# Kernel tuning notes

Hardware: AMD Instinct MI355X
Metric: run time of the kernel (lower is better)

The kernel has to match this reference:

```python
import jax, jax.numpy as jnp
import numpy as np

N_HEADS = 16

def setup_inputs() -> dict:
    key = jax.random.key(0)
    qkv = jax.random.normal(key, (4, 3072, 2048), dtype=jnp.float32)
    return {"qkv": qkv}

def reference(qkv) -> jnp.ndarray:
    bs, width, length = qkv.shape
    ch = width // (3 * N_HEADS)
    # [bs*H, 3*ch, T] -> split into q, k, v each [bs*H, ch, T]
    qkv_r = qkv.reshape(bs * N_HEADS, 3 * ch, length)
    q, k, v = qkv_r[:, :ch], qkv_r[:, ch:2 * ch], qkv_r[:, 2 * ch:]
    scale = 1.0 / jnp.sqrt(jnp.sqrt(jnp.float32(ch)))
    # scores: [bs*H, T, T]
    weight = jnp.einsum('bct,bcs->bts', q * scale, k * scale)
    weight = jax.nn.softmax(weight.astype(jnp.float32), axis=-1).astype(weight.dtype)
    a = jnp.einsum('bts,bcs->bct', weight, v)  # [bs*H, ch, T]
    return a.reshape(bs, N_HEADS * ch, length)
```

## Files before the change

### kernel.cpp

```cpp
#include <hip/hip_runtime.h>

namespace {

constexpr int D  = 64;
constexpr int T  = 2048;
constexpr int TQ = 64;
constexpr int NT = T / 64;
constexpr float SCL = 0.125f * 1.44269504088896340736f;

constexpr size_t QP_OFF  = (size_t)64 * 32 * 8192;
constexpr size_t WS_NEED = ((size_t)64 * 32 * 8192 + (size_t)64 * 32 * 4096) * 2;

typedef __bf16 bf16x8 __attribute__((ext_vector_type(8)));
typedef float  f32x4  __attribute__((ext_vector_type(4)));
typedef unsigned short u16x4 __attribute__((ext_vector_type(4)));
typedef unsigned short u16x8 __attribute__((ext_vector_type(8)));
typedef unsigned int   u32x2 __attribute__((ext_vector_type(2)));
typedef short          s16x4 __attribute__((ext_vector_type(4)));

__device__ inline unsigned short f2bf(float f) {
    unsigned int u = __builtin_bit_cast(unsigned int, f);
    u += 0x7FFFu + ((u >> 16) & 1u);
    return (unsigned short)(u >> 16);
}

__device__ inline unsigned int pkbf(float a, float b) {
#if __has_builtin(__builtin_amdgcn_cvt_pk_bf16_f32)
    auto r = __builtin_amdgcn_cvt_pk_bf16_f32(a, b);
    static_assert(sizeof(r) == 4, "cvt_pk_bf16 size");
    return __builtin_bit_cast(unsigned int, r);
#else
    return (unsigned int)f2bf(a) | ((unsigned int)f2bf(b) << 16);
#endif
}

__device__ inline int frag_off(int row, int c0) {
    int g = (c0 >> 3) ^ ((row >> 1) & 7);
    return row * 64 + g * 8;
}

__device__ inline void async_cp16(const void* g, void* l) {
    __builtin_amdgcn_global_load_lds(
        (const __attribute__((address_space(1))) unsigned int*)g,
        (__attribute__((address_space(3))) unsigned int*)l, 16, 0, 0);
}

__global__ __launch_bounds__(256)
void prepass(const float* __restrict__ qkv, unsigned short* __restrict__ ws) {
    const int tile = blockIdx.x, h = blockIdx.y, z = blockIdx.z;
    const int tid = threadIdx.x;
    const float* src = qkv + (size_t)h * 3 * D * T + (size_t)z * D * T + tile * 64;
    __shared__ unsigned short L[4096];

    if (z == 2) {
        unsigned short* dst = ws + (size_t)(h * 32 + tile) * 8192 + 4096;
        const int c = tid >> 2, g = tid & 3;
        const int sg = g ^ ((c >> 2) & 3);
        #pragma unroll
        for (int wq = 0; wq < 4; wq++) {
            f32x4 a = *(const f32x4*)(src + (size_t)c * T + wq * 16 + sg * 4);
            u16x4 wv = { f2bf(a[0]), f2bf(a[1]), f2bf(a[2]), f2bf(a[3]) };
            *(u16x4*)(dst + wq * 1024 + tid * 4) = wv;
        }
    } else {
        const float m = (z == 0) ? SCL : 1.0f;
        const int c0 = (tid >> 4) * 4, s4 = tid & 15;
        float fr[4][4];
        #pragma unroll
        for (int r = 0; r < 4; r++)
            *(f32x4*)fr[r] = *(const f32x4*)(src + (size_t)(c0 + r) * T + s4 * 4);
        #pragma unroll
        for (int j = 0; j < 4; j++) {
            int trow = s4 * 4 + j;
            u16x4 wv = { f2bf(fr[0][j] * m), f2bf(fr[1][j] * m),
                         f2bf(fr[2][j] * m), f2bf(fr[3][j] * m) };
            *(u16x4*)(L + frag_off(trow, c0) + (c0 & 7)) = wv;
        }
        __syncthreads();
        unsigned short* dst = (z == 0)
            ? ws + QP_OFF + (size_t)(h * 32 + tile) * 4096
            : ws + (size_t)(h * 32 + tile) * 8192;
        #pragma unroll
        for (int i = 0; i < 2; i++)
            *(u16x8*)(dst + tid * 16 + i * 8) = *(const u16x8*)(L + tid * 16 + i * 8);
    }
}


#define STAGE(J, B)                                                          \
  { const char* g = kvb + (size_t)(J) * 16384;                               \
    char* lk = wbase + (B) * 4096;                                           \
    async_cp16(g,               lk);                                         \
    async_cp16(g + 1024,        lk + 1024);                                  \
    async_cp16(g + 8192,        lk + 2048);                                  \
    async_cp16(g + 8192 + 1024, lk + 3072); }

#define BODY(KT, B, DO_STAGE, WAITIMM)                                       \
  {                                                                          \
    __builtin_amdgcn_s_waitcnt(0xC07F);           \
    if (DO_STAGE) STAGE((KT) + 1, (B) ^ 1)                                   \
    __builtin_amdgcn_s_waitcnt(WAITIMM);       \
    bf16x8 aK0 = *(const bf16x8*)aKp[B][0];                                  \
    bf16x8 aK1 = *(const bf16x8*)aKp[B][1];                                  \
    s16x4 aV0 = *(const s16x4*)aVp[B][0];                                    \
    s16x4 aV1 = *(const s16x4*)aVp[B][1];                                    \
    s16x4 aV2 = *(const s16x4*)aVp[B][2];                                    \
    s16x4 aV3 = *(const s16x4*)aVp[B][3];                                    \
    f32x4 acc_s[4];                                                          \
    _Pragma("unroll")                                                        \
    for (int ti = 0; ti < 4; ti++)                                           \
      acc_s[ti] = __builtin_amdgcn_mfma_f32_16x16x32_bf16(                   \
          aK0, bQ[ti][0], ZF, 0, 0, 0);                                      \
    _Pragma("unroll")                                                        \
    for (int ti = 0; ti < 4; ti++)                                           \
      acc_s[ti] = __builtin_amdgcn_mfma_f32_16x16x32_bf16(                   \
          aK1, bQ[ti][1], acc_s[ti], 0, 0, 0);                               \
    s16x4 bP[4];                                                             \
    _Pragma("unroll")                                                        \
    for (int ti = 0; ti < 4; ti++) {                                         \
      float p0 = __builtin_amdgcn_exp2f(acc_s[ti][0]);                       \
      float p1 = __builtin_amdgcn_exp2f(acc_s[ti][1]);                       \
      float p2 = __builtin_amdgcn_exp2f(acc_s[ti][2]);                       \
      float p3 = __builtin_amdgcn_exp2f(acc_s[ti][3]);                       \
      l_acc[ti] += (p0 + p1) + (p2 + p3);                                    \
      u32x2 pk = { pkbf(p0, p1), pkbf(p2, p3) };                             \
      bP[ti] = __builtin_bit_cast(s16x4, pk);                                \
    }                                                                        \
    _Pragma("unroll")                                                        \
    for (int ti = 0; ti < 4; ti++) {                                         \
      acc_o[0][ti] = __builtin_amdgcn_mfma_f32_16x16x16bf16_1k(              \
          aV0, bP[ti], acc_o[0][ti], 0, 0, 0);                               \
      acc_o[1][ti] = __builtin_amdgcn_mfma_f32_16x16x16bf16_1k(              \
          aV1, bP[ti], acc_o[1][ti], 0, 0, 0);                               \
      acc_o[2][ti] = __builtin_amdgcn_mfma_f32_16x16x16bf16_1k(              \
          aV2, bP[ti], acc_o[2][ti], 0, 0, 0);                               \
      acc_o[3][ti] = __builtin_amdgcn_mfma_f32_16x16x16bf16_1k(              \
          aV3, bP[ti], acc_o[3][ti], 0, 0, 0);                               \
    }                                                                        \
  }

__global__ __launch_bounds__(256, 3)
void attn_main(const unsigned short* __restrict__ ws, float* __restrict__ out) {
    const int h  = blockIdx.x;
    const int qt = blockIdx.y;
    const int t0 = qt * TQ;
    const int tid  = threadIdx.x;
    const int lane = tid & 63;
    const int w    = tid >> 6;
    const int ln   = lane & 15, q4 = lane >> 4;

    __shared__ char  sbuf[32768];
    __shared__ float lbuf[256];
    char* wbase = sbuf + w * 8192;

    const unsigned short* qtile = ws + QP_OFF + (size_t)(h * 32 + qt) * 4096;
    bf16x8 bQ[4][2];
    #pragma unroll
    for (int ti = 0; ti < 4; ti++)
        #pragma unroll
        for (int kc = 0; kc < 2; kc++)
            bQ[ti][kc] = *(const bf16x8*)(qtile + frag_off(ti * 16 + ln, kc * 32 + q4 * 8));

    const unsigned short* aKp[2][2];
    const unsigned short* aVp[2][4];
    const int vsw = (q4 ^ ((ln >> 2) & 3)) * 4;
    #pragma unroll
    for (int b = 0; b < 2; b++) {
        const unsigned short* base = (const unsigned short*)(wbase + b * 4096);
        #pragma unroll
        for (int kc = 0; kc < 2; kc++)
            aKp[b][kc] = base + frag_off(ln, kc * 32 + q4 * 8);
        #pragma unroll
        for (int ci = 0; ci < 4; ci++)
            aVp[b][ci] = base + 1024 + (16 * ci + ln) * 16 + vsw;
    }
    const char* kvb = (const char*)ws + (size_t)(h * 32) * 16384
                      + (size_t)w * 2048 + lane * 16;
    const f32x4 ZF = {0.f, 0.f, 0.f, 0.f};

    f32x4 acc_o[4][4];
    #pragma unroll
    for (int ci = 0; ci < 4; ci++)
        #pragma unroll
        for (int ti = 0; ti < 4; ti++) acc_o[ci][ti] = ZF;
    float l_acc[4] = {0.f, 0.f, 0.f, 0.f};

    STAGE(0, 0)

    #pragma unroll 1
    for (int m = 0; m < 15; m++) {
        BODY(2 * m,     0, 1, 0x0F74)
        BODY(2 * m + 1, 1, 1, 0x0F74)
    }
    BODY(30, 0, 1, 0x0F74)
    BODY(31, 1, 0, 0x0F70)

    __syncthreads();
    #pragma unroll
    for (int ti = 0; ti < 4; ti++) {
        float s = l_acc[ti];
        s += __shfl_xor(s, 16, 64);
        s += __shfl_xor(s, 32, 64);
        if (q4 == 0) lbuf[w * 64 + ti * 16 + ln] = s;
    }
    float* slots = (float*)sbuf;
    #pragma unroll
    for (int q = 0; q < 4; q++)
        if ((q ^ w) & 1) {
            float* dst = slots + w * 2048 + (q >> 1) * 1024;
            #pragma unroll
            for (int ti = 0; ti < 4; ti++)
                *(f32x4*)(dst + ti * 256 + lane * 4) = acc_o[q][ti];
        }
    __syncthreads();
    #pragma unroll
    for (int q = 0; q < 4; q++)
        if (!((q ^ w) & 1)) {
            const float* srcp = slots + (w ^ 1) * 2048 + (q >> 1) * 1024;
            #pragma unroll
            for (int ti = 0; ti < 4; ti++)
                acc_o[q][ti] += *(const f32x4*)(srcp + ti * 256 + lane * 4);
        }
    __syncthreads();
    #pragma unroll
    for (int q = 0; q < 4; q++)
        if (((q ^ w) & 3) == 2) {
            float* dst = slots + w * 2048;
            #pragma unroll
            for (int ti = 0; ti < 4; ti++)
                *(f32x4*)(dst + ti * 256 + lane * 4) = acc_o[q][ti];
        }
    __syncthreads();
    #pragma unroll
    for (int q = 0; q < 4; q++)
        if (q == w) {
            const float* srcp = slots + (w ^ 2) * 2048;
            float linv[4];
            #pragma unroll
            for (int ti = 0; ti < 4; ti++) {
                int tt = ti * 16 + ln;
                linv[ti] = 1.0f / (lbuf[tt] + lbuf[64 + tt] +
                                   lbuf[128 + tt] + lbuf[192 + tt]);
                acc_o[q][ti] += *(const f32x4*)(srcp + ti * 256 + lane * 4);
            }
            float* ob = out + (size_t)h * D * T + t0;
            #pragma unroll
            for (int ti = 0; ti < 4; ti++)
                #pragma unroll
                for (int rr = 0; rr < 4; rr++) {
                    int c = 16 * w + q4 * 4 + rr;
                    ob[(size_t)c * T + ti * 16 + ln] = acc_o[q][ti][rr] * linv[ti];
                }
        }
}

__device__ inline bf16x8 frag8(const unsigned short* p, int row, int c0) {
    return *(const bf16x8*)(p + frag_off(row, c0));
}

__global__ __launch_bounds__(256)
void attn_fallback(const float* __restrict__ qkv, float* __restrict__ out) {
    const int h     = blockIdx.y;
    const int t0    = blockIdx.x * TQ;
    const int tid   = threadIdx.x;
    const int lane  = tid & 63;
    const int strip = tid >> 6;
    const int ln    = lane & 15;
    const int q4    = lane >> 4;

    __shared__ unsigned short Qs[TQ * D];
    __shared__ unsigned short Ks[64 * D];
    __shared__ unsigned short Vs[D * 64];
    __shared__ unsigned short Pss[TQ * 64];
    __shared__ float l_lds[TQ];

    const float* qb = qkv + (size_t)h * 3 * D * T;
    const float* kb = qb + (size_t)D * T;
    const float* vb = qb + (size_t)(2 * D) * T;
    const int s4 = tid & 15;
    const int c0 = (tid >> 4) * 4;
    {
        float fr[4][4];
        #pragma unroll
        for (int r = 0; r < 4; r++)
            *(f32x4*)fr[r] = *(const f32x4*)(qb + (size_t)(c0 + r) * T + t0 + s4 * 4);
        #pragma unroll
        for (int j = 0; j < 4; j++) {
            int trow = s4 * 4 + j;
            u16x4 wv = { f2bf(fr[0][j]), f2bf(fr[1][j]), f2bf(fr[2][j]), f2bf(fr[3][j]) };
            *(u16x4*)(Qs + frag_off(trow, c0) + (c0 & 7)) = wv;
        }
    }
    __syncthreads();
    const int arow = strip * 16 + ln;
    const int kg   = q4 * 8;
    const bf16x8 aq0 = frag8(Qs, arow, kg);
    const bf16x8 aq1 = frag8(Qs, arow, 32 + kg);
    f32x4 acc_o[4];
    #pragma unroll
    for (int m = 0; m < 4; m++) acc_o[m] = (f32x4){0.f, 0.f, 0.f, 0.f};
    float l_acc[4] = {0.f, 0.f, 0.f, 0.f};
    constexpr float S2 = 0.125f * 1.44269504088896340736f;
    for (int kt = 0; kt < NT; kt++) {
        const int s0 = kt * 64;
        float kr[4][4], vr[4][4];
        #pragma unroll
        for (int r = 0; r < 4; r++)
            *(f32x4*)kr[r] = *(const f32x4*)(kb + (size_t)(c0 + r) * T + s0 + s4 * 4);
        #pragma unroll
        for (int r = 0; r < 4; r++)
            *(f32x4*)vr[r] = *(const f32x4*)(vb + (size_t)(c0 + r) * T + s0 + s4 * 4);
        __syncthreads();
        #pragma unroll
        for (int j = 0; j < 4; j++) {
            int srow = s4 * 4 + j;
            u16x4 wk = { f2bf(kr[0][j]), f2bf(kr[1][j]), f2bf(kr[2][j]), f2bf(kr[3][j]) };
            *(u16x4*)(Ks + frag_off(srow, c0) + (c0 & 7)) = wk;
        }
        #pragma unroll
        for (int r = 0; r < 4; r++) {
            int row = c0 + r, cc = s4 * 4;
            u16x4 wv = { f2bf(vr[r][0]), f2bf(vr[r][1]), f2bf(vr[r][2]), f2bf(vr[r][3]) };
            *(u16x4*)(Vs + frag_off(row, cc) + (cc & 7)) = wv;
        }
        __syncthreads();
        f32x4 accs[4];
        #pragma unroll
        for (int ns = 0; ns < 4; ns++) {
            bf16x8 b0 = frag8(Ks, ns * 16 + ln, kg);
            bf16x8 b1 = frag8(Ks, ns * 16 + ln, 32 + kg);
            f32x4 z = {0.f, 0.f, 0.f, 0.f};
            z = __builtin_amdgcn_mfma_f32_16x16x32_bf16(aq0, b0, z, 0, 0, 0);
            z = __builtin_amdgcn_mfma_f32_16x16x32_bf16(aq1, b1, z, 0, 0, 0);
            accs[ns] = z;
        }
        #pragma unroll
        for (int ns = 0; ns < 4; ns++) {
            int scol = ns * 16 + ln;
            #pragma unroll
            for (int r = 0; r < 4; r++) {
                float p = __builtin_amdgcn_exp2f(accs[ns][r] * S2);
                l_acc[r] += p;
                int trow = strip * 16 + q4 * 4 + r;
                int g = ((scol >> 3) ^ ((trow >> 1) & 7));
                Pss[trow * 64 + g * 8 + (scol & 7)] = f2bf(p);
            }
        }
        bf16x8 bp0 = frag8(Pss, arow, kg);
        bf16x8 bp1 = frag8(Pss, arow, 32 + kg);
        #pragma unroll
        for (int ms = 0; ms < 4; ms++) {
            bf16x8 av0 = frag8(Vs, ms * 16 + ln, kg);
            bf16x8 av1 = frag8(Vs, ms * 16 + ln, 32 + kg);
            acc_o[ms] = __builtin_amdgcn_mfma_f32_16x16x32_bf16(av0, bp0, acc_o[ms], 0, 0, 0);
            acc_o[ms] = __builtin_amdgcn_mfma_f32_16x16x32_bf16(av1, bp1, acc_o[ms], 0, 0, 0);
        }
    }
    #pragma unroll
    for (int r = 0; r < 4; r++) {
        float s = l_acc[r];
        s += __shfl_xor(s, 1, 64);
        s += __shfl_xor(s, 2, 64);
        s += __shfl_xor(s, 4, 64);
        s += __shfl_xor(s, 8, 64);
        if (ln == 0) l_lds[strip * 16 + q4 * 4 + r] = s;
    }
    const float linv = 1.0f / l_lds[strip * 16 + ln];
    const int tg = t0 + strip * 16 + ln;
    float* ob = out + (size_t)h * D * T;
    #pragma unroll
    for (int ms = 0; ms < 4; ms++)
        #pragma unroll
        for (int r = 0; r < 4; r++) {
            int c = ms * 16 + q4 * 4 + r;
            ob[(size_t)c * T + tg] = acc_o[ms][r] * linv;
        }
}

}

extern "C" void kernel_launch(void* const* d_in, const int* in_sizes, int n_in,
                              void* d_out, int out_size, void* d_ws, size_t ws_size,
                              hipStream_t stream) {
    const float* qkv = (const float*)d_in[0];
    float* out = (float*)d_out;
    if (ws_size >= WS_NEED) {
        prepass<<<dim3(32, 64, 3), 256, 0, stream>>>(qkv, (unsigned short*)d_ws);
        attn_main<<<dim3(64, 32), 256, 0, stream>>>((const unsigned short*)d_ws, out);
    } else {
        attn_fallback<<<dim3(32, 64), 256, 0, stream>>>(qkv, out);
    }
}
```

Measured before the change: 254.3 us.

## Load Q directly in attention kernel and deepen K/V prefetch pipeline

The prepass no longer converts Q. The attention kernel now loads its Q tile from fp32 input, scales and converts it to bf16, and stages it through shared memory, which removes a workspace round-trip and one third of the prepass grid. The K/V loop now issues global-to-LDS copies two tiles ahead and register-prefetches the next tile's fragments. It also interleaves the QK MFMA, exp and PV MFMA per pair of query subtiles, with a sched_barrier in between. The row-sum buffer is folded into the reused shared slots, at the cost of more register pressure and harder occupancy at 3 waves/SIMD.

```diff
diff --git a/kernel.cpp b/kernel.cpp
--- a/kernel.cpp
+++ b/kernel.cpp
@@ -8,8 +8,7 @@
 constexpr int NT = T / 64;
 constexpr float SCL = 0.125f * 1.44269504088896340736f;
 
-constexpr size_t QP_OFF  = (size_t)64 * 32 * 8192;
-constexpr size_t WS_NEED = ((size_t)64 * 32 * 8192 + (size_t)64 * 32 * 4096) * 2;
+constexpr size_t WS_NEED = (size_t)64 * 32 * 8192 * 2;
 
 typedef __bf16 bf16x8 __attribute__((ext_vector_type(8)));
 typedef float  f32x4  __attribute__((ext_vector_type(4)));
@@ -47,12 +46,12 @@
 
 __global__ __launch_bounds__(256)
 void prepass(const float* __restrict__ qkv, unsigned short* __restrict__ ws) {
-    const int tile = blockIdx.x, h = blockIdx.y, z = blockIdx.z;
+    const int tile = blockIdx.x, h = blockIdx.y, zz = blockIdx.z;
     const int tid = threadIdx.x;
-    const float* src = qkv + (size_t)h * 3 * D * T + (size_t)z * D * T + tile * 64;
+    const float* src = qkv + (size_t)h * 3 * D * T + (size_t)(zz + 1) * D * T + tile * 64;
     __shared__ unsigned short L[4096];
 
-    if (z == 2) {
+    if (zz == 1) {
         unsigned short* dst = ws + (size_t)(h * 32 + tile) * 8192 + 4096;
         const int c = tid >> 2, g = tid & 3;
         const int sg = g ^ ((c >> 2) & 3);
@@ -63,7 +62,6 @@
             *(u16x4*)(dst + wq * 1024 + tid * 4) = wv;
         }
     } else {
-        const float m = (z == 0) ? SCL : 1.0f;
         const int c0 = (tid >> 4) * 4, s4 = tid & 15;
         float fr[4][4];
         #pragma unroll
@@ -72,14 +70,12 @@
         #pragma unroll
         for (int j = 0; j < 4; j++) {
             int trow = s4 * 4 + j;
-            u16x4 wv = { f2bf(fr[0][j] * m), f2bf(fr[1][j] * m),
-                         f2bf(fr[2][j] * m), f2bf(fr[3][j] * m) };
+            u16x4 wv = { f2bf(fr[0][j]), f2bf(fr[1][j]),
+                         f2bf(fr[2][j]), f2bf(fr[3][j]) };
             *(u16x4*)(L + frag_off(trow, c0) + (c0 & 7)) = wv;
         }
         __syncthreads();
-        unsigned short* dst = (z == 0)
-            ? ws + QP_OFF + (size_t)(h * 32 + tile) * 4096
-            : ws + (size_t)(h * 32 + tile) * 8192;
+        unsigned short* dst = ws + (size_t)(h * 32 + tile) * 8192;
         #pragma unroll
         for (int i = 0; i < 2; i++)
             *(u16x8*)(dst + tid * 16 + i * 8) = *(const u16x8*)(L + tid * 16 + i * 8);
@@ -95,52 +91,65 @@
     async_cp16(g + 8192,        lk + 2048);                                  \
     async_cp16(g + 8192 + 1024, lk + 3072); }
 
-#define BODY(KT, B, DO_STAGE, WAITIMM)                                       \
+#define PREF(NB)                                                             \
+  { aK[NB][0] = *(const bf16x8*)(wbase + (NB) * 4096 + kOff0);               \
+    aK[NB][1] = *(const bf16x8*)(wbase + (NB) * 4096 + kOff1);               \
+    aV[NB][0] = *(const s16x4*)(wbase + (NB) * 4096 + vBase);                \
+    aV[NB][1] = *(const s16x4*)(wbase + (NB) * 4096 + vBase + 512);          \
+    aV[NB][2] = *(const s16x4*)(wbase + (NB) * 4096 + vBase + 1024);         \
+    aV[NB][3] = *(const s16x4*)(wbase + (NB) * 4096 + vBase + 1536); }
+
+#define BODY(KT, B, DO_STAGE, DO_PREF, WAITIMM)                              \
   {                                                                          \
     __builtin_amdgcn_s_waitcnt(0xC07F);           \
-    if (DO_STAGE) STAGE((KT) + 1, (B) ^ 1)                                   \
-    __builtin_amdgcn_s_waitcnt(WAITIMM);       \
-    bf16x8 aK0 = *(const bf16x8*)aKp[B][0];                                  \
-    bf16x8 aK1 = *(const bf16x8*)aKp[B][1];                                  \
-    s16x4 aV0 = *(const s16x4*)aVp[B][0];                                    \
-    s16x4 aV1 = *(const s16x4*)aVp[B][1];                                    \
-    s16x4 aV2 = *(const s16x4*)aVp[B][2];                                    \
-    s16x4 aV3 = *(const s16x4*)aVp[B][3];                                    \
-    f32x4 acc_s[4];                                                          \
+    if (DO_STAGE) STAGE((KT) + 2, B)                                         \
+    if (DO_PREF) {                                                           \
+      __builtin_amdgcn_s_waitcnt(WAITIMM);   \
+      PREF((B) ^ 1)                                                          \
+    }                                                                        \
+    __builtin_amdgcn_sched_barrier(0);   \
     _Pragma("unroll")                                                        \
-    for (int ti = 0; ti < 4; ti++)                                           \
-      acc_s[ti] = __builtin_amdgcn_mfma_f32_16x16x32_bf16(                   \
-          aK0, bQ[ti][0], ZF, 0, 0, 0);                                      \
-    _Pragma("unroll")                                                        \
-    for (int ti = 0; ti < 4; ti++)                                           \
-      acc_s[ti] = __builtin_amdgcn_mfma_f32_16x16x32_bf16(                   \
-          aK1, bQ[ti][1], acc_s[ti], 0, 0, 0);                               \
-    s16x4 bP[4];                                                             \
-    _Pragma("unroll")                                                        \
-    for (int ti = 0; ti < 4; ti++) {                                         \
-      float p0 = __builtin_amdgcn_exp2f(acc_s[ti][0]);                       \
-      float p1 = __builtin_amdgcn_exp2f(acc_s[ti][1]);                       \
-      float p2 = __builtin_amdgcn_exp2f(acc_s[ti][2]);                       \
-      float p3 = __builtin_amdgcn_exp2f(acc_s[ti][3]);                       \
-      l_acc[ti] += (p0 + p1) + (p2 + p3);                                    \
-      u32x2 pk = { pkbf(p0, p1), pkbf(p2, p3) };                             \
-      bP[ti] = __builtin_bit_cast(s16x4, pk);                                \
-    }                                                                        \
-    _Pragma("unroll")                                                        \
-    for (int ti = 0; ti < 4; ti++) {                                         \
-      acc_o[0][ti] = __builtin_amdgcn_mfma_f32_16x16x16bf16_1k(              \
-          aV0, bP[ti], acc_o[0][ti], 0, 0, 0);                               \
-      acc_o[1][ti] = __builtin_amdgcn_mfma_f32_16x16x16bf16_1k(              \
-          aV1, bP[ti], acc_o[1][ti], 0, 0, 0);                               \
-      acc_o[2][ti] = __builtin_amdgcn_mfma_f32_16x16x16bf16_1k(              \
-          aV2, bP[ti], acc_o[2][ti], 0, 0, 0);                               \
-      acc_o[3][ti] = __builtin_amdgcn_mfma_f32_16x16x16bf16_1k(              \
-          aV3, bP[ti], acc_o[3][ti], 0, 0, 0);                               \
+    for (int tp = 0; tp < 2; tp++) {     \
+      f32x4 s0 = __builtin_amdgcn_mfma_f32_16x16x32_bf16(                    \
+          aK[B][0], bQ[2 * tp][0], ZF, 0, 0, 0);                             \
+      s0 = __builtin_amdgcn_mfma_f32_16x16x32_bf16(                          \
+          aK[B][1], bQ[2 * tp][1], s0, 0, 0, 0);                             \
+      f32x4 s1 = __builtin_amdgcn_mfma_f32_16x16x32_bf16(                    \
+          aK[B][0], bQ[2 * tp + 1][0], ZF, 0, 0, 0);                         \
+      s1 = __builtin_amdgcn_mfma_f32_16x16x32_bf16(                          \
+          aK[B][1], bQ[2 * tp + 1][1], s1, 0, 0, 0);                         \
+      s16x4 bP0, bP1;                                                        \
+      {                                                                      \
+        float p0 = __builtin_amdgcn_exp2f(s0[0]);                            \
+        float p1 = __builtin_amdgcn_exp2f(s0[1]);                            \
+        float p2 = __builtin_amdgcn_exp2f(s0[2]);                            \
+        float p3 = __builtin_amdgcn_exp2f(s0[3]);                            \
+        l_acc[2 * tp] += (p0 + p1) + (p2 + p3);                              \
+        u32x2 pk = { pkbf(p0, p1), pkbf(p2, p3) };                           \
+        bP0 = __builtin_bit_cast(s16x4, pk);                                 \
+      }                                                                      \
+      {                                                                      \
+        float p0 = __builtin_amdgcn_exp2f(s1[0]);                            \
+        float p1 = __builtin_amdgcn_exp2f(s1[1]);                            \
+        float p2 = __builtin_amdgcn_exp2f(s1[2]);                            \
+        float p3 = __builtin_amdgcn_exp2f(s1[3]);                            \
+        l_acc[2 * tp + 1] += (p0 + p1) + (p2 + p3);                          \
+        u32x2 pk = { pkbf(p0, p1), pkbf(p2, p3) };                           \
+        bP1 = __builtin_bit_cast(s16x4, pk);                                 \
+      }                                                                      \
+      _Pragma("unroll")                                                      \
+      for (int ci = 0; ci < 4; ci++) {                                       \
+        acc_o[ci][2 * tp]     = __builtin_amdgcn_mfma_f32_16x16x16bf16_1k(   \
+            aV[B][ci], bP0, acc_o[ci][2 * tp], 0, 0, 0);                     \
+        acc_o[ci][2 * tp + 1] = __builtin_amdgcn_mfma_f32_16x16x16bf16_1k(   \
+            aV[B][ci], bP1, acc_o[ci][2 * tp + 1], 0, 0, 0);                 \
+      }                                                                      \
     }                                                                        \
   }
 
 __global__ __launch_bounds__(256, 3)
-void attn_main(const unsigned short* __restrict__ ws, float* __restrict__ out) {
+void attn_main(const unsigned short* __restrict__ ws,
+               const float* __restrict__ qkv, float* __restrict__ out) {
     const int h  = blockIdx.x;
     const int qt = blockIdx.y;
     const int t0 = qt * TQ;
@@ -149,35 +158,47 @@
     const int w    = tid >> 6;
     const int ln   = lane & 15, q4 = lane >> 4;
 
-    __shared__ char  sbuf[32768];
-    __shared__ float lbuf[256];
+    __shared__ char sbuf[32768];
     char* wbase = sbuf + w * 8192;
-
-    const unsigned short* qtile = ws + QP_OFF + (size_t)(h * 32 + qt) * 4096;
-    bf16x8 bQ[4][2];
-    #pragma unroll
-    for (int ti = 0; ti < 4; ti++)
-        #pragma unroll
-        for (int kc = 0; kc < 2; kc++)
-            bQ[ti][kc] = *(const bf16x8*)(qtile + frag_off(ti * 16 + ln, kc * 32 + q4 * 8));
-
-    const unsigned short* aKp[2][2];
-    const unsigned short* aVp[2][4];
-    const int vsw = (q4 ^ ((ln >> 2) & 3)) * 4;
-    #pragma unroll
-    for (int b = 0; b < 2; b++) {
-        const unsigned short* base = (const unsigned short*)(wbase + b * 4096);
-        #pragma unroll
-        for (int kc = 0; kc < 2; kc++)
-            aKp[b][kc] = base + frag_off(ln, kc * 32 + q4 * 8);
-        #pragma unroll
-        for (int ci = 0; ci < 4; ci++)
-            aVp[b][ci] = base + 1024 + (16 * ci + ln) * 16 + vsw;
-    }
+    unsigned short* S16 = (unsigned short*)sbuf;
+
+    const float* qsrc = qkv + (size_t)h * 3 * D * T + t0;
+    const int c0 = (tid >> 4) * 4, s4 = tid & 15;
+    float fr[4][4];
+    #pragma unroll
+    for (int r = 0; r < 4; r++)
+        *(f32x4*)fr[r] = *(const f32x4*)(qsrc + (size_t)(c0 + r) * T + s4 * 4);
+
     const char* kvb = (const char*)ws + (size_t)(h * 32) * 16384
                       + (size_t)w * 2048 + lane * 16;
+    STAGE(0, 0)
+
+    #pragma unroll
+    for (int j = 0; j < 4; j++) {
+        int trow = s4 * 4 + j;
+        int g = (c0 >> 3) ^ ((trow >> 1) & 7);
+        u16x4 wv = { f2bf(fr[0][j] * SCL), f2bf(fr[1][j] * SCL),
+                     f2bf(fr[2][j] * SCL), f2bf(fr[3][j] * SCL) };
+        *(u16x4*)(S16 + (trow >> 4) * 4096 + 2048 + (trow & 15) * 64 + g * 8 + (c0 & 7)) = wv;
+    }
+    __syncthreads();
+    bf16x8 bQ[4][2];
+    #pragma unroll
+    for (int ti = 0; ti < 4; ti++)
+        #pragma unroll
+        for (int kc = 0; kc < 2; kc++) {
+            int cc = kc * 32 + q4 * 8;
+            int g = (cc >> 3) ^ ((ln >> 1) & 7);
+            bQ[ti][kc] = *(const bf16x8*)(S16 + ti * 4096 + 2048 + ln * 64 + g * 8);
+        }
+    __syncthreads();
+
+    const int kOff0 = 2 * frag_off(ln, q4 * 8);
+    const int kOff1 = 2 * frag_off(ln, 32 + q4 * 8);
+    const int vsw   = (q4 ^ ((ln >> 2) & 3)) * 4;
+    const int vBase = 2048 + 32 * ln + 2 * vsw;
+
     const f32x4 ZF = {0.f, 0.f, 0.f, 0.f};
-
     f32x4 acc_o[4][4];
     #pragma unroll
     for (int ci = 0; ci < 4; ci++)
@@ -185,24 +206,28 @@
         for (int ti = 0; ti < 4; ti++) acc_o[ci][ti] = ZF;
     float l_acc[4] = {0.f, 0.f, 0.f, 0.f};
 
-    STAGE(0, 0)
+    bf16x8 aK[2][2];
+    s16x4  aV[2][4];
+    PREF(0)
+    STAGE(1, 1)
 
     #pragma unroll 1
     for (int m = 0; m < 15; m++) {
-        BODY(2 * m,     0, 1, 0x0F74)
-        BODY(2 * m + 1, 1, 1, 0x0F74)
-    }
-    BODY(30, 0, 1, 0x0F74)
-    BODY(31, 1, 0, 0x0F70)
-
-    __syncthreads();
+        BODY(2 * m,     0, 1, 1, 0x0F74)
+        BODY(2 * m + 1, 1, 1, 1, 0x0F74)
+    }
+    BODY(30, 0, 0, 1, 0x0F70)
+    BODY(31, 1, 0, 0, 0x0F70)
+
+    float lv[4];
     #pragma unroll
     for (int ti = 0; ti < 4; ti++) {
         float s = l_acc[ti];
         s += __shfl_xor(s, 16, 64);
         s += __shfl_xor(s, 32, 64);
-        if (q4 == 0) lbuf[w * 64 + ti * 16 + ln] = s;
-    }
+        lv[ti] = s;
+    }
+    __syncthreads();
     float* slots = (float*)sbuf;
     #pragma unroll
     for (int q = 0; q < 4; q++)
@@ -230,6 +255,11 @@
             for (int ti = 0; ti < 4; ti++)
                 *(f32x4*)(dst + ti * 256 + lane * 4) = acc_o[q][ti];
         }
+    if (q4 == 0) {
+        #pragma unroll
+        for (int ti = 0; ti < 4; ti++)
+            slots[w * 2048 + 1024 + ti * 16 + ln] = lv[ti];
+    }
     __syncthreads();
     #pragma unroll
     for (int q = 0; q < 4; q++)
@@ -239,8 +269,8 @@
             #pragma unroll
             for (int ti = 0; ti < 4; ti++) {
                 int tt = ti * 16 + ln;
-                linv[ti] = 1.0f / (lbuf[tt] + lbuf[64 + tt] +
-                                   lbuf[128 + tt] + lbuf[192 + tt]);
+                linv[ti] = 1.0f / (slots[1024 + tt] + slots[2048 + 1024 + tt] +
+                                   slots[4096 + 1024 + tt] + slots[6144 + 1024 + tt]);
                 acc_o[q][ti] += *(const f32x4*)(srcp + ti * 256 + lane * 4);
             }
             float* ob = out + (size_t)h * D * T + t0;
@@ -385,8 +415,8 @@
     const float* qkv = (const float*)d_in[0];
     float* out = (float*)d_out;
     if (ws_size >= WS_NEED) {
-        prepass<<<dim3(32, 64, 3), 256, 0, stream>>>(qkv, (unsigned short*)d_ws);
-        attn_main<<<dim3(64, 32), 256, 0, stream>>>((const unsigned short*)d_ws, out);
+        prepass<<<dim3(32, 64, 2), 256, 0, stream>>>(qkv, (unsigned short*)d_ws);
+        attn_main<<<dim3(64, 32), 256, 0, stream>>>((const unsigned short*)d_ws, qkv, out);
     } else {
         attn_fallback<<<dim3(32, 64), 256, 0, stream>>>(qkv, out);
     }
```

Measured after the change: 293.5 us. 1.15x slower.

## Fuse Q conversion into attention kernel and triple-buffer K/V staging

Applied to the files above, without the earlier changes.

The prepass no longer converts Q to bf16. Instead, attn_main loads its fp32 Q tile directly, scales and converts it, and moves it into registers through LDS. This removes a third of the prepass work and the Q workspace round trip. The K/V async staging also goes from double to triple buffering, prefetching two tiles ahead, which raises LDS to 48KB per block and may limit occupancy under the 3-blocks launch bound.

```diff
diff --git a/kernel.cpp b/kernel.cpp
--- a/kernel.cpp
+++ b/kernel.cpp
@@ -8,8 +8,7 @@
 constexpr int NT = T / 64;
 constexpr float SCL = 0.125f * 1.44269504088896340736f;
 
-constexpr size_t QP_OFF  = (size_t)64 * 32 * 8192;
-constexpr size_t WS_NEED = ((size_t)64 * 32 * 8192 + (size_t)64 * 32 * 4096) * 2;
+constexpr size_t WS_NEED = (size_t)64 * 32 * 8192 * 2;
 
 typedef __bf16 bf16x8 __attribute__((ext_vector_type(8)));
 typedef float  f32x4  __attribute__((ext_vector_type(4)));
@@ -47,12 +46,12 @@
 
 __global__ __launch_bounds__(256)
 void prepass(const float* __restrict__ qkv, unsigned short* __restrict__ ws) {
-    const int tile = blockIdx.x, h = blockIdx.y, z = blockIdx.z;
+    const int tile = blockIdx.x, h = blockIdx.y, zz = blockIdx.z;
     const int tid = threadIdx.x;
-    const float* src = qkv + (size_t)h * 3 * D * T + (size_t)z * D * T + tile * 64;
+    const float* src = qkv + (size_t)h * 3 * D * T + (size_t)(zz + 1) * D * T + tile * 64;
     __shared__ unsigned short L[4096];
 
-    if (z == 2) {
+    if (zz == 1) {
         unsigned short* dst = ws + (size_t)(h * 32 + tile) * 8192 + 4096;
         const int c = tid >> 2, g = tid & 3;
         const int sg = g ^ ((c >> 2) & 3);
@@ -63,7 +62,6 @@
             *(u16x4*)(dst + wq * 1024 + tid * 4) = wv;
         }
     } else {
-        const float m = (z == 0) ? SCL : 1.0f;
         const int c0 = (tid >> 4) * 4, s4 = tid & 15;
         float fr[4][4];
         #pragma unroll
@@ -72,14 +70,12 @@
         #pragma unroll
         for (int j = 0; j < 4; j++) {
             int trow = s4 * 4 + j;
-            u16x4 wv = { f2bf(fr[0][j] * m), f2bf(fr[1][j] * m),
-                         f2bf(fr[2][j] * m), f2bf(fr[3][j] * m) };
+            u16x4 wv = { f2bf(fr[0][j]), f2bf(fr[1][j]),
+                         f2bf(fr[2][j]), f2bf(fr[3][j]) };
             *(u16x4*)(L + frag_off(trow, c0) + (c0 & 7)) = wv;
         }
         __syncthreads();
-        unsigned short* dst = (z == 0)
-            ? ws + QP_OFF + (size_t)(h * 32 + tile) * 4096
-            : ws + (size_t)(h * 32 + tile) * 8192;
+        unsigned short* dst = ws + (size_t)(h * 32 + tile) * 8192;
         #pragma unroll
         for (int i = 0; i < 2; i++)
             *(u16x8*)(dst + tid * 16 + i * 8) = *(const u16x8*)(L + tid * 16 + i * 8);
@@ -95,17 +91,17 @@
     async_cp16(g + 8192,        lk + 2048);                                  \
     async_cp16(g + 8192 + 1024, lk + 3072); }
 
-#define BODY(KT, B, DO_STAGE, WAITIMM)                                       \
+#define BODY(KT, B, SB, DO_STAGE, WAITIMM)                                   \
   {                                                                          \
     __builtin_amdgcn_s_waitcnt(0xC07F);           \
-    if (DO_STAGE) STAGE((KT) + 1, (B) ^ 1)                                   \
+    if (DO_STAGE) STAGE((KT) + 2, SB)                                        \
     __builtin_amdgcn_s_waitcnt(WAITIMM);       \
-    bf16x8 aK0 = *(const bf16x8*)aKp[B][0];                                  \
-    bf16x8 aK1 = *(const bf16x8*)aKp[B][1];                                  \
-    s16x4 aV0 = *(const s16x4*)aVp[B][0];                                    \
-    s16x4 aV1 = *(const s16x4*)aVp[B][1];                                    \
-    s16x4 aV2 = *(const s16x4*)aVp[B][2];                                    \
-    s16x4 aV3 = *(const s16x4*)aVp[B][3];                                    \
+    bf16x8 aK0 = *(const bf16x8*)(aK0p + (B) * 4096);                        \
+    bf16x8 aK1 = *(const bf16x8*)(aK1p + (B) * 4096);                        \
+    s16x4 aV0 = *(const s16x4*)(aVp + (B) * 4096);                           \
+    s16x4 aV1 = *(const s16x4*)(aVp + (B) * 4096 + 512);                     \
+    s16x4 aV2 = *(const s16x4*)(aVp + (B) * 4096 + 1024);                    \
+    s16x4 aV3 = *(const s16x4*)(aVp + (B) * 4096 + 1536);                    \
     f32x4 acc_s[4];                                                          \
     _Pragma("unroll")                                                        \
     for (int ti = 0; ti < 4; ti++)                                           \
@@ -140,7 +136,8 @@
   }
 
 __global__ __launch_bounds__(256, 3)
-void attn_main(const unsigned short* __restrict__ ws, float* __restrict__ out) {
+void attn_main(const unsigned short* __restrict__ ws,
+               const float* __restrict__ qkv, float* __restrict__ out) {
     const int h  = blockIdx.x;
     const int qt = blockIdx.y;
     const int t0 = qt * TQ;
@@ -149,35 +146,48 @@
     const int w    = tid >> 6;
     const int ln   = lane & 15, q4 = lane >> 4;
 
-    __shared__ char  sbuf[32768];
-    __shared__ float lbuf[256];
-    char* wbase = sbuf + w * 8192;
-
-    const unsigned short* qtile = ws + QP_OFF + (size_t)(h * 32 + qt) * 4096;
-    bf16x8 bQ[4][2];
-    #pragma unroll
-    for (int ti = 0; ti < 4; ti++)
-        #pragma unroll
-        for (int kc = 0; kc < 2; kc++)
-            bQ[ti][kc] = *(const bf16x8*)(qtile + frag_off(ti * 16 + ln, kc * 32 + q4 * 8));
-
-    const unsigned short* aKp[2][2];
-    const unsigned short* aVp[2][4];
-    const int vsw = (q4 ^ ((ln >> 2) & 3)) * 4;
-    #pragma unroll
-    for (int b = 0; b < 2; b++) {
-        const unsigned short* base = (const unsigned short*)(wbase + b * 4096);
-        #pragma unroll
-        for (int kc = 0; kc < 2; kc++)
-            aKp[b][kc] = base + frag_off(ln, kc * 32 + q4 * 8);
-        #pragma unroll
-        for (int ci = 0; ci < 4; ci++)
-            aVp[b][ci] = base + 1024 + (16 * ci + ln) * 16 + vsw;
-    }
+    __shared__ char sbuf[49152];
+    char* wbase = sbuf + w * 12288;
+    unsigned short* S16 = (unsigned short*)sbuf;
+
+    const float* qsrc = qkv + (size_t)h * 3 * D * T + t0;
+    const int c0 = (tid >> 4) * 4, s4 = tid & 15;
+    float fr[4][4];
+    #pragma unroll
+    for (int r = 0; r < 4; r++)
+        *(f32x4*)fr[r] = *(const f32x4*)(qsrc + (size_t)(c0 + r) * T + s4 * 4);
+
     const char* kvb = (const char*)ws + (size_t)(h * 32) * 16384
                       + (size_t)w * 2048 + lane * 16;
+    STAGE(0, 0)
+    STAGE(1, 1)
+
+    #pragma unroll
+    for (int j = 0; j < 4; j++) {
+        int trow = s4 * 4 + j;
+        int g = (c0 >> 3) ^ ((trow >> 1) & 7);
+        u16x4 wv = { f2bf(fr[0][j] * SCL), f2bf(fr[1][j] * SCL),
+                     f2bf(fr[2][j] * SCL), f2bf(fr[3][j] * SCL) };
+        *(u16x4*)(S16 + (trow >> 4) * 6144 + 4096 + (trow & 15) * 64 + g * 8 + (c0 & 7)) = wv;
+    }
+    __syncthreads();
+    bf16x8 bQ[4][2];
+    #pragma unroll
+    for (int ti = 0; ti < 4; ti++)
+        #pragma unroll
+        for (int kc = 0; kc < 2; kc++) {
+            int cc = kc * 32 + q4 * 8;
+            int g = (cc >> 3) ^ ((ln >> 1) & 7);
+            bQ[ti][kc] = *(const bf16x8*)(S16 + ti * 6144 + 4096 + ln * 64 + g * 8);
+        }
+    __syncthreads();
+
+    const char* aK0p = wbase + 2 * frag_off(ln, q4 * 8);
+    const char* aK1p = wbase + 2 * frag_off(ln, 32 + q4 * 8);
+    const int   vsw  = (q4 ^ ((ln >> 2) & 3)) * 4;
+    const char* aVp  = wbase + 2048 + 32 * ln + 2 * vsw;
+
     const f32x4 ZF = {0.f, 0.f, 0.f, 0.f};
-
     f32x4 acc_o[4][4];
     #pragma unroll
     for (int ci = 0; ci < 4; ci++)
@@ -185,24 +195,24 @@
         for (int ti = 0; ti < 4; ti++) acc_o[ci][ti] = ZF;
     float l_acc[4] = {0.f, 0.f, 0.f, 0.f};
 
-    STAGE(0, 0)
-
     #pragma unroll 1
-    for (int m = 0; m < 15; m++) {
-        BODY(2 * m,     0, 1, 0x0F74)
-        BODY(2 * m + 1, 1, 1, 0x0F74)
-    }
-    BODY(30, 0, 1, 0x0F74)
-    BODY(31, 1, 0, 0x0F70)
-
-    __syncthreads();
+    for (int m = 0; m < 10; m++) {
+        BODY(3 * m,     0, 2, 1, 0x0F78)
+        BODY(3 * m + 1, 1, 0, 1, 0x0F78)
+        BODY(3 * m + 2, 2, 1, 1, 0x0F78)
+    }
+    BODY(30, 0, 0, 0, 0x0F74)
+    BODY(31, 1, 0, 0, 0x0F70)
+
+    float lv[4];
     #pragma unroll
     for (int ti = 0; ti < 4; ti++) {
         float s = l_acc[ti];
         s += __shfl_xor(s, 16, 64);
         s += __shfl_xor(s, 32, 64);
-        if (q4 == 0) lbuf[w * 64 + ti * 16 + ln] = s;
-    }
+        lv[ti] = s;
+    }
+    __syncthreads();
     float* slots = (float*)sbuf;
     #pragma unroll
     for (int q = 0; q < 4; q++)
@@ -230,6 +240,11 @@
             for (int ti = 0; ti < 4; ti++)
                 *(f32x4*)(dst + ti * 256 + lane * 4) = acc_o[q][ti];
         }
+    if (q4 == 0) {
+        #pragma unroll
+        for (int ti = 0; ti < 4; ti++)
+            slots[w * 2048 + 1024 + ti * 16 + ln] = lv[ti];
+    }
     __syncthreads();
     #pragma unroll
     for (int q = 0; q < 4; q++)
@@ -239,8 +254,8 @@
             #pragma unroll
             for (int ti = 0; ti < 4; ti++) {
                 int tt = ti * 16 + ln;
-                linv[ti] = 1.0f / (lbuf[tt] + lbuf[64 + tt] +
-                                   lbuf[128 + tt] + lbuf[192 + tt]);
+                linv[ti] = 1.0f / (slots[1024 + tt] + slots[2048 + 1024 + tt] +
+                                   slots[4096 + 1024 + tt] + slots[6144 + 1024 + tt]);
                 acc_o[q][ti] += *(const f32x4*)(srcp + ti * 256 + lane * 4);
             }
             float* ob = out + (size_t)h * D * T + t0;
@@ -385,8 +400,8 @@
     const float* qkv = (const float*)d_in[0];
     float* out = (float*)d_out;
     if (ws_size >= WS_NEED) {
-        prepass<<<dim3(32, 64, 3), 256, 0, stream>>>(qkv, (unsigned short*)d_ws);
-        attn_main<<<dim3(64, 32), 256, 0, stream>>>((const unsigned short*)d_ws, out);
+        prepass<<<dim3(32, 64, 2), 256, 0, stream>>>(qkv, (unsigned short*)d_ws);
+        attn_main<<<dim3(64, 32), 256, 0, stream>>>((const unsigned short*)d_ws, qkv, out);
     } else {
         attn_fallback<<<dim3(32, 64), 256, 0, stream>>>(qkv, out);
     }
```

Result: slower. 362.8 us (+42.7%).

## Split attention work by query rows across waves with shared KV staging

Applied to the files above, without the earlier changes.

Before, each wave took a slice of the key sequence for all 64 queries, which needed a four-way LDS reduction of the output accumulators at the end. Now each wave owns 16 query rows and walks all keys. The block cooperatively stages shared K/V tiles into LDS, double-buffered with block barriers. This removes the cross-wave reduction, shrinks per-thread accumulator registers and raises the occupancy hint to 4. In exchange it adds a block-wide barrier at every key tile and each wave does less MFMA work per LDS read.

```diff
diff --git a/kernel.cpp b/kernel.cpp
--- a/kernel.cpp
+++ b/kernel.cpp
@@ -89,57 +89,53 @@
 
 #define STAGE(J, B)                                                          \
   { const char* g = kvb + (size_t)(J) * 16384;                               \
-    char* lk = wbase + (B) * 4096;                                           \
-    async_cp16(g,               lk);                                         \
-    async_cp16(g + 1024,        lk + 1024);                                  \
-    async_cp16(g + 8192,        lk + 2048);                                  \
-    async_cp16(g + 8192 + 1024, lk + 3072); }
+    char* lk = lbase + (B) * 16384;                                          \
+    async_cp16(g,         lk);                                               \
+    async_cp16(g + 4096,  lk + 4096);                                        \
+    async_cp16(g + 8192,  lk + 8192);                                        \
+    async_cp16(g + 12288, lk + 12288); }
 
 #define BODY(KT, B, DO_STAGE, WAITIMM)                                       \
   {                                                                          \
-    __builtin_amdgcn_s_waitcnt(0xC07F);           \
-    if (DO_STAGE) STAGE((KT) + 1, (B) ^ 1)                                   \
-    __builtin_amdgcn_s_waitcnt(WAITIMM);       \
-    bf16x8 aK0 = *(const bf16x8*)aKp[B][0];                                  \
-    bf16x8 aK1 = *(const bf16x8*)aKp[B][1];                                  \
-    s16x4 aV0 = *(const s16x4*)aVp[B][0];                                    \
-    s16x4 aV1 = *(const s16x4*)aVp[B][1];                                    \
-    s16x4 aV2 = *(const s16x4*)aVp[B][2];                                    \
-    s16x4 aV3 = *(const s16x4*)aVp[B][3];                                    \
-    f32x4 acc_s[4];                                                          \
+    __builtin_amdgcn_s_waitcnt(WAITIMM);         \
+    __builtin_amdgcn_s_barrier();             \
+    __builtin_amdgcn_sched_barrier(0);          \
     _Pragma("unroll")                                                        \
-    for (int ti = 0; ti < 4; ti++)                                           \
-      acc_s[ti] = __builtin_amdgcn_mfma_f32_16x16x32_bf16(                   \
-          aK0, bQ[ti][0], ZF, 0, 0, 0);                                      \
-    _Pragma("unroll")                                                        \
-    for (int ti = 0; ti < 4; ti++)                                           \
-      acc_s[ti] = __builtin_amdgcn_mfma_f32_16x16x32_bf16(                   \
-          aK1, bQ[ti][1], acc_s[ti], 0, 0, 0);                               \
-    s16x4 bP[4];                                                             \
-    _Pragma("unroll")                                                        \
-    for (int ti = 0; ti < 4; ti++) {                                         \
-      float p0 = __builtin_amdgcn_exp2f(acc_s[ti][0]);                       \
-      float p1 = __builtin_amdgcn_exp2f(acc_s[ti][1]);                       \
-      float p2 = __builtin_amdgcn_exp2f(acc_s[ti][2]);                       \
-      float p3 = __builtin_amdgcn_exp2f(acc_s[ti][3]);                       \
-      l_acc[ti] += (p0 + p1) + (p2 + p3);                                    \
+    for (int q = 0; q < 4; q++) {                                            \
+      const char* kb = sbuf + (B) * 16384 + q * 2048;                        \
+      const char* vb = sbuf + (B) * 16384 + 8192 + q * 2048;                 \
+      bf16x8 aK0 = *(const bf16x8*)(kb + aK0o);                              \
+      bf16x8 aK1 = *(const bf16x8*)(kb + aK1o);                              \
+      s16x4 aV0 = *(const s16x4*)(vb + aVo);                                 \
+      s16x4 aV1 = *(const s16x4*)(vb + aVo + 512);                           \
+      s16x4 aV2 = *(const s16x4*)(vb + aVo + 1024);                          \
+      s16x4 aV3 = *(const s16x4*)(vb + aVo + 1536);                          \
+      f32x4 s = __builtin_amdgcn_mfma_f32_16x16x32_bf16(aK0, bQ0, ZF, 0,0,0);\
+      s = __builtin_amdgcn_mfma_f32_16x16x32_bf16(aK1, bQ1, s, 0, 0, 0);     \
+      float p0 = __builtin_amdgcn_exp2f(s[0]);                               \
+      float p1 = __builtin_amdgcn_exp2f(s[1]);                               \
+      float p2 = __builtin_amdgcn_exp2f(s[2]);                               \
+      float p3 = __builtin_amdgcn_exp2f(s[3]);                               \
+      l_acc += (p0 + p1) + (p2 + p3);                                        \
       u32x2 pk = { pkbf(p0, p1), pkbf(p2, p3) };                             \
-      bP[ti] = __builtin_bit_cast(s16x4, pk);                                \
+      s16x4 bP = __builtin_bit_cast(s16x4, pk);                              \
+      acc_o[0] = __builtin_amdgcn_mfma_f32_16x16x16bf16_1k(                  \
+          aV0, bP, acc_o[0], 0, 0, 0);                                       \
+      acc_o[1] = __builtin_amdgcn_mfma_f32_16x16x16bf16_1k(                  \
+          aV1, bP, acc_o[1], 0, 0, 0);                                       \
+      acc_o[2] = __builtin_amdgcn_mfma_f32_16x16x16bf16_1k(                  \
+          aV2, bP, acc_o[2], 0, 0, 0);                                       \
+      acc_o[3] = __builtin_amdgcn_mfma_f32_16x16x16bf16_1k(                  \
+          aV3, bP, acc_o[3], 0, 0, 0);                                       \
     }                                                                        \
-    _Pragma("unroll")                                                        \
-    for (int ti = 0; ti < 4; ti++) {                                         \
-      acc_o[0][ti] = __builtin_amdgcn_mfma_f32_16x16x16bf16_1k(              \
-          aV0, bP[ti], acc_o[0][ti], 0, 0, 0);                               \
-      acc_o[1][ti] = __builtin_amdgcn_mfma_f32_16x16x16bf16_1k(              \
-          aV1, bP[ti], acc_o[1][ti], 0, 0, 0);                               \
-      acc_o[2][ti] = __builtin_amdgcn_mfma_f32_16x16x16bf16_1k(              \
-          aV2, bP[ti], acc_o[2][ti], 0, 0, 0);                               \
-      acc_o[3][ti] = __builtin_amdgcn_mfma_f32_16x16x16bf16_1k(              \
-          aV3, bP[ti], acc_o[3][ti], 0, 0, 0);                               \
+    if (DO_STAGE) {                                                          \
+      __builtin_amdgcn_s_waitcnt(0xC07F);        \
+      __builtin_amdgcn_s_barrier();           \
+      STAGE((KT) + 2, B)                                                     \
     }                                                                        \
   }
 
-__global__ __launch_bounds__(256, 3)
+__global__ __launch_bounds__(256, 4)
 void attn_main(const unsigned short* __restrict__ ws, float* __restrict__ out) {
     const int h  = blockIdx.x;
     const int qt = blockIdx.y;
@@ -149,109 +145,44 @@
     const int w    = tid >> 6;
     const int ln   = lane & 15, q4 = lane >> 4;
 
-    __shared__ char  sbuf[32768];
-    __shared__ float lbuf[256];
-    char* wbase = sbuf + w * 8192;
+    __shared__ char sbuf[32768];
+    char* lbase = sbuf + w * 1024;
+
+    const int aK0o = 2 * frag_off(ln, q4 * 8);
+    const int aK1o = 2 * frag_off(ln, 32 + q4 * 8);
+    const int aVo  = 32 * ln + 2 * ((q4 ^ ((ln >> 2) & 3)) * 4);
 
     const unsigned short* qtile = ws + QP_OFF + (size_t)(h * 32 + qt) * 4096;
-    bf16x8 bQ[4][2];
-    #pragma unroll
-    for (int ti = 0; ti < 4; ti++)
-        #pragma unroll
-        for (int kc = 0; kc < 2; kc++)
-            bQ[ti][kc] = *(const bf16x8*)(qtile + frag_off(ti * 16 + ln, kc * 32 + q4 * 8));
-
-    const unsigned short* aKp[2][2];
-    const unsigned short* aVp[2][4];
-    const int vsw = (q4 ^ ((ln >> 2) & 3)) * 4;
-    #pragma unroll
-    for (int b = 0; b < 2; b++) {
-        const unsigned short* base = (const unsigned short*)(wbase + b * 4096);
-        #pragma unroll
-        for (int kc = 0; kc < 2; kc++)
-            aKp[b][kc] = base + frag_off(ln, kc * 32 + q4 * 8);
-        #pragma unroll
-        for (int ci = 0; ci < 4; ci++)
-            aVp[b][ci] = base + 1024 + (16 * ci + ln) * 16 + vsw;
-    }
+    bf16x8 bQ0 = *(const bf16x8*)(qtile + frag_off(16 * w + ln, q4 * 8));
+    bf16x8 bQ1 = *(const bf16x8*)(qtile + frag_off(16 * w + ln, 32 + q4 * 8));
+
     const char* kvb = (const char*)ws + (size_t)(h * 32) * 16384
-                      + (size_t)w * 2048 + lane * 16;
+                      + w * 1024 + lane * 16;
+    STAGE(0, 0)
+    STAGE(1, 1)
+
     const f32x4 ZF = {0.f, 0.f, 0.f, 0.f};
-
-    f32x4 acc_o[4][4];
-    #pragma unroll
-    for (int ci = 0; ci < 4; ci++)
-        #pragma unroll
-        for (int ti = 0; ti < 4; ti++) acc_o[ci][ti] = ZF;
-    float l_acc[4] = {0.f, 0.f, 0.f, 0.f};
-
-    STAGE(0, 0)
+    f32x4 acc_o[4] = {ZF, ZF, ZF, ZF};
+    float l_acc = 0.f;
 
     #pragma unroll 1
     for (int m = 0; m < 15; m++) {
         BODY(2 * m,     0, 1, 0x0F74)
         BODY(2 * m + 1, 1, 1, 0x0F74)
     }
-    BODY(30, 0, 1, 0x0F74)
+    BODY(30, 0, 0, 0x0F74)
     BODY(31, 1, 0, 0x0F70)
 
-    __syncthreads();
+    float sl = l_acc;
+    sl += __shfl_xor(sl, 16, 64);
+    sl += __shfl_xor(sl, 32, 64);
+    const float linv = 1.0f / sl;
+    float* ob = out + (size_t)h * D * T + t0 + 16 * w + ln;
     #pragma unroll
-    for (int ti = 0; ti < 4; ti++) {
-        float s = l_acc[ti];
-        s += __shfl_xor(s, 16, 64);
-        s += __shfl_xor(s, 32, 64);
-        if (q4 == 0) lbuf[w * 64 + ti * 16 + ln] = s;
-    }
-    float* slots = (float*)sbuf;
-    #pragma unroll
-    for (int q = 0; q < 4; q++)
-        if ((q ^ w) & 1) {
-            float* dst = slots + w * 2048 + (q >> 1) * 1024;
-            #pragma unroll
-            for (int ti = 0; ti < 4; ti++)
-                *(f32x4*)(dst + ti * 256 + lane * 4) = acc_o[q][ti];
-        }
-    __syncthreads();
-    #pragma unroll
-    for (int q = 0; q < 4; q++)
-        if (!((q ^ w) & 1)) {
-            const float* srcp = slots + (w ^ 1) * 2048 + (q >> 1) * 1024;
-            #pragma unroll
-            for (int ti = 0; ti < 4; ti++)
-                acc_o[q][ti] += *(const f32x4*)(srcp + ti * 256 + lane * 4);
-        }
-    __syncthreads();
-    #pragma unroll
-    for (int q = 0; q < 4; q++)
-        if (((q ^ w) & 3) == 2) {
-            float* dst = slots + w * 2048;
-            #pragma unroll
-            for (int ti = 0; ti < 4; ti++)
-                *(f32x4*)(dst + ti * 256 + lane * 4) = acc_o[q][ti];
-        }
-    __syncthreads();
-    #pragma unroll
-    for (int q = 0; q < 4; q++)
-        if (q == w) {
-            const float* srcp = slots + (w ^ 2) * 2048;
-            float linv[4];
-            #pragma unroll
-            for (int ti = 0; ti < 4; ti++) {
-                int tt = ti * 16 + ln;
-                linv[ti] = 1.0f / (lbuf[tt] + lbuf[64 + tt] +
-                                   lbuf[128 + tt] + lbuf[192 + tt]);
-                acc_o[q][ti] += *(const f32x4*)(srcp + ti * 256 + lane * 4);
-            }
-            float* ob = out + (size_t)h * D * T + t0;
-            #pragma unroll
-            for (int ti = 0; ti < 4; ti++)
-                #pragma unroll
-                for (int rr = 0; rr < 4; rr++) {
-                    int c = 16 * w + q4 * 4 + rr;
-                    ob[(size_t)c * T + ti * 16 + ln] = acc_o[q][ti][rr] * linv[ti];
-                }
-        }
+    for (int ci = 0; ci < 4; ci++)
+        #pragma unroll
+        for (int rr = 0; rr < 4; rr++)
+            ob[(size_t)(16 * ci + q4 * 4 + rr) * T] = acc_o[ci][rr] * linv;
 }
 
 __device__ inline bf16x8 frag8(const unsigned short* p, int row, int c0) {
```

Result: no change. 254.1 us (-0.1%).
